# Performance work log

Measured on AMD Instinct MI355X. Metric: run time of the kernel, lower is better.

The kernel has to match this reference:

```python
import jax, jax.numpy as jnp
import numpy as np

B, H, S, D = 4, 16, 2048, 64


def setup_inputs() -> dict:
    key = jax.random.key(0)
    kq, kk, kv = jax.random.split(key, 3)
    q = jax.random.normal(kq, (B, H, S, D), dtype=jnp.float32)
    k = jax.random.normal(kk, (B, H, S, D), dtype=jnp.float32)
    v = jax.random.normal(kv, (B, H, S, D), dtype=jnp.float32)
    return {"q": q, "k": k, "v": v, "num_k": 170}


def reference(q, k, v, num_k):
    d_tensor = k.shape[-1]
    # [B,H,S,S] score matrix
    score = jnp.einsum("bhqd,bhkd->bhqk", q, k) / jnp.sqrt(jnp.float32(d_tensor))
    nk = min(int(num_k), k.shape[2])
    if nk:
        # kth-largest value per query row acts as threshold
        top_vals = jax.lax.top_k(score, nk)[0]          # [B,H,S,nk]
        thresh = top_vals[..., -1:]                      # [B,H,S,1]
        score = jnp.where(score < thresh, jnp.float32(-1e18), score)
    attn = jax.nn.softmax(score, axis=-1)
    return jnp.einsum("bhqk,bhkd->bhqd", attn, v)
```

## Files before the change

kernel.cpp:

```cpp
#include <hip/hip_runtime.h>
#include <math.h>

#define S_LEN 2048
#define DHEAD 64
#define NBINS 512
#define BPL (NBINS / 64)
#define CANDMAX 48
#define NBH 64
#define NROWS (NBH * S_LEN)
#define VT_BYTES (64ull * DHEAD * S_LEN * 2)

typedef _Float16 f16x8 __attribute__((ext_vector_type(8)));
typedef _Float16 f16x4 __attribute__((ext_vector_type(4)));
typedef float    f32x4 __attribute__((ext_vector_type(4)));

__global__ __launch_bounds__(256)
void prep_vt(const float* __restrict__ V, _Float16* __restrict__ VT) {
  const int bh  = (int)blockIdx.x >> 3;
  const int dg8 = (int)blockIdx.x & 7;
  const int t   = (int)threadIdx.x;
  const int dim = dg8 * 8 + (t >> 5);
  const int kc  = t & 31;
  const float* Vb = V + (size_t)bh * (S_LEN * DHEAD);
  _Float16* VTb = VT + ((size_t)bh * DHEAD + dim) * S_LEN;
  for (int i = 0; i < 8; ++i) {
    int key0 = (kc + i * 32) * 8;
    f16x8 h;
    #pragma unroll
    for (int j = 0; j < 8; ++j)
      h[j] = (_Float16)Vb[(size_t)(key0 + j) * DHEAD + dim];
    *(f16x8*)(VTb + key0) = h;
  }
}

__global__ __launch_bounds__(256, 4)
void qk_kernel(const float* __restrict__ Q, const float* __restrict__ K,
               float* __restrict__ Sws, int row0) {
  __shared__ __align__(16) char kbuf[32768];
  f16x8* Khw = (f16x8*)kbuf;
  f16x8* Klw = (f16x8*)(kbuf + 16384);

  const int tid  = (int)threadIdx.x;
  const int lane = tid & 63;
  const int wid  = tid >> 6;
  const int nxl  = (int)gridDim.x >> 3;
  const int xcd  = (int)blockIdx.x & 7;
  const int lb   = (int)blockIdx.x >> 3;
  const int rb   = lb >> 3;
  const int kb   = lb & 7;
  const int rowl = xcd * (nxl * 8) + rb * 64 + wid * 16;
  const int rowg = row0 + rowl;
  const int bh   = rowg >> 11;
  const int key0 = kb * 256;

  const int g = lane >> 4;
  const int m = lane & 15;

  f16x8 a_hi0, a_lo0, a_hi1, a_lo1;
  {
    const float* Qrow = Q + (size_t)(rowg + m) * DHEAD;
    float4 qa = *(const float4*)(Qrow + g * 8);
    float4 qb = *(const float4*)(Qrow + g * 8 + 4);
    float4 qc = *(const float4*)(Qrow + 32 + g * 8);
    float4 qd = *(const float4*)(Qrow + 32 + g * 8 + 4);
    float x[16] = {qa.x,qa.y,qa.z,qa.w, qb.x,qb.y,qb.z,qb.w,
                   qc.x,qc.y,qc.z,qc.w, qd.x,qd.y,qd.z,qd.w};
    #pragma unroll
    for (int j = 0; j < 8; ++j) {
      _Float16 h0 = (_Float16)x[j];
      a_hi0[j] = h0;  a_lo0[j] = (_Float16)(x[j] - (float)h0);
      _Float16 h1 = (_Float16)x[8 + j];
      a_hi1[j] = h1;  a_lo1[j] = (_Float16)(x[8 + j] - (float)h1);
    }
  }

  const float* Kb = K + (size_t)bh * (S_LEN * DHEAD);
  float* Srow = Sws + (size_t)rowl * S_LEN;

  const int skey  = tid >> 1;
  const int shalf = tid & 1;
  const int ssw   = skey & 7;

  float4 pf[8];
  {
    const float4* kr = (const float4*)(Kb + (size_t)(key0 + skey) * DHEAD + shalf * 32);
    #pragma unroll
    for (int j = 0; j < 8; ++j) pf[j] = kr[j];
  }

  #pragma unroll
  for (int t = 0; t < 2; ++t) {
    #pragma unroll
    for (int jj = 0; jj < 4; ++jj) {
      float x[8] = {pf[2*jj].x, pf[2*jj].y, pf[2*jj].z, pf[2*jj].w,
                    pf[2*jj+1].x, pf[2*jj+1].y, pf[2*jj+1].z, pf[2*jj+1].w};
      f16x8 hi, lo;
      #pragma unroll
      for (int j = 0; j < 8; ++j) {
        _Float16 h = (_Float16)x[j];
        hi[j] = h;
        lo[j] = (_Float16)(x[j] - (float)h);
      }
      int c = shalf * 4 + jj;
      Khw[skey * 8 + (c ^ ssw)] = hi;
      Klw[skey * 8 + (c ^ ssw)] = lo;
    }
    if (t + 1 < 2) {
      const float4* kr = (const float4*)(Kb + (size_t)(key0 + 128 + skey) * DHEAD + shalf * 32);
      #pragma unroll
      for (int j = 0; j < 8; ++j) pf[j] = kr[j];
    }
    __syncthreads();

    const f16x8* Kh = (const f16x8*)kbuf;
    const f16x8* Kl = (const f16x8*)(kbuf + 16384);
    int slot0 = ( g      ^ (m & 7));
    int slot1 = ((4 + g) ^ (m & 7));
    #pragma unroll
    for (int p = 0; p < 8; ++p) {
      int keyr = p * 16 + m;
      f16x8 b_hi0 = Kh[keyr * 8 + slot0];
      f16x8 b_hi1 = Kh[keyr * 8 + slot1];
      f16x8 b_lo0 = Kl[keyr * 8 + slot0];
      f16x8 b_lo1 = Kl[keyr * 8 + slot1];
      f32x4 acc = {0.f, 0.f, 0.f, 0.f};
      acc = __builtin_amdgcn_mfma_f32_16x16x32_f16(a_hi0, b_hi0, acc, 0, 0, 0);
      acc = __builtin_amdgcn_mfma_f32_16x16x32_f16(a_hi1, b_hi1, acc, 0, 0, 0);
      acc = __builtin_amdgcn_mfma_f32_16x16x32_f16(a_hi0, b_lo0, acc, 0, 0, 0);
      acc = __builtin_amdgcn_mfma_f32_16x16x32_f16(a_hi1, b_lo1, acc, 0, 0, 0);
      acc = __builtin_amdgcn_mfma_f32_16x16x32_f16(a_lo0, b_hi0, acc, 0, 0, 0);
      acc = __builtin_amdgcn_mfma_f32_16x16x32_f16(a_lo1, b_hi1, acc, 0, 0, 0);
      acc = __builtin_amdgcn_mfma_f32_16x16x32_f16(a_lo0, b_lo0, acc, 0, 0, 0);
      acc = __builtin_amdgcn_mfma_f32_16x16x32_f16(a_lo1, b_lo1, acc, 0, 0, 0);
      int col = key0 + t * 128 + p * 16 + m;
      #pragma unroll
      for (int rg = 0; rg < 4; ++rg)
        __builtin_nontemporal_store(acc[rg] * 0.125f,
            &Srow[(size_t)(g * 4 + rg) * S_LEN + col]);
    }
    __syncthreads();
  }
}

__global__ __launch_bounds__(512, 4)
void selmm_kernel(const float* __restrict__ Sws, const _Float16* __restrict__ VT,
                  const int* __restrict__ nkp, float* __restrict__ Out, int row0) {
  __shared__ unsigned histS[8][NBINS];
  __shared__ float candS[8][CANDMAX];
  __shared__ unsigned candCnt[8];
  __shared__ float psumS[16];
  __shared__ __align__(16) char pbuf[8192];
  __shared__ __align__(16) float4 redS[4][64];

  const int tid  = (int)threadIdx.x;
  const int lane = tid & 63;
  const int wid  = tid >> 6;
  const int nxl  = (int)gridDim.x >> 3;
  const int xcd  = (int)blockIdx.x & 7;
  const int lbk  = (int)blockIdx.x >> 3;
  const int rowlb = xcd * (nxl * 16) + lbk * 16;
  const int rowgb = row0 + rowlb;
  const int bh    = rowgb >> 11;

  int nk = nkp[0];
  if (nk > S_LEN) nk = S_LEN;

  unsigned* hw = histS[wid];
  float sarr[2][32];
  float thr2[2], vmx2[2];

  #pragma unroll
  for (int rr = 0; rr < 2; ++rr) {
    const int rloc = wid * 2 + rr;
    {
      const f32x4* S4 = (const f32x4*)(Sws + (size_t)(rowlb + rloc) * S_LEN);
      #pragma unroll
      for (int j = 0; j < 8; ++j) {
        f32x4 v4 = __builtin_nontemporal_load(S4 + j * 64 + lane);
        sarr[rr][j*4+0] = v4[0]; sarr[rr][j*4+1] = v4[1];
        sarr[rr][j*4+2] = v4[2]; sarr[rr][j*4+3] = v4[3];
      }
    }

    float vmax = -INFINITY, vmin = INFINITY;
    #pragma unroll
    for (int q = 0; q < 32; ++q) {
      vmax = fmaxf(vmax, sarr[rr][q]); vmin = fminf(vmin, sarr[rr][q]);
    }
    #pragma unroll
    for (int off = 32; off >= 1; off >>= 1) {
      vmax = fmaxf(vmax, __shfl_xor(vmax, off));
      vmin = fminf(vmin, __shfl_xor(vmin, off));
    }

    float thresh = -INFINITY;
    if (nk > 0) {
      float range = vmax - vmin;
      float scale = (range > 0.f) ? ((float)NBINS / range) : 0.f;
      float boff  = vmin * scale;

      #pragma unroll
      for (int i2 = 0; i2 < BPL; ++i2) hw[(i2 << 6) | lane] = 0u;
      #pragma unroll
      for (int q = 0; q < 32; ++q) {
        int bb = (int)fmaf(sarr[rr][q], scale, -boff);
        bb = bb < 0 ? 0 : (bb > NBINS - 1 ? NBINS - 1 : bb);
        atomicAdd(&hw[((bb & 7) << 6) | (bb >> 3)], 1u);
      }

      unsigned A = 0;
      #pragma unroll
      for (int i2 = 0; i2 < BPL; ++i2) A += hw[(i2 << 6) | lane];
      unsigned ssum = A;
      #pragma unroll
      for (int off = 1; off <= 32; off <<= 1) {
        unsigned u = (unsigned)__shfl_down((int)ssum, off);
        if (lane + off < 64) ssum += u;
      }
      unsigned cum = ssum - A;
      int bsel = -1; int mloc = 0; int nbloc = 0;
      #pragma unroll
      for (int i2 = BPL - 1; i2 >= 0; --i2) {
        unsigned c0 = cum; cum += hw[(i2 << 6) | lane];
        if (bsel < 0 && c0 < (unsigned)nk && cum >= (unsigned)nk) {
          bsel = (lane << 3) | i2; mloc = nk - (int)c0; nbloc = (int)(cum - c0);
        }
      }
      unsigned long long fm = __ballot(bsel >= 0);
      int srcl = __ffsll(fm) - 1;
      bsel = __shfl(bsel, srcl);
      int mth  = __shfl(mloc, srcl);
      int nbin = __shfl(nbloc, srcl);

      if (nbin <= CANDMAX) {
        if (lane == 0) candCnt[wid] = 0u;
        __builtin_amdgcn_wave_barrier();
        #pragma unroll
        for (int q = 0; q < 32; ++q) {
          int bb = (int)fmaf(sarr[rr][q], scale, -boff);
          bb = bb < 0 ? 0 : (bb > NBINS - 1 ? NBINS - 1 : bb);
          if (bb == bsel) {
            unsigned ix = atomicAdd(&candCnt[wid], 1u);
            if (ix < CANDMAX) candS[wid][ix] = sarr[rr][q];
          }
        }
        __builtin_amdgcn_wave_barrier();
        float prev = INFINITY, kth = -INFINITY;
        int got = 0, guard = 0;
        while (got < mth && guard++ <= CANDMAX) {
          float best = -INFINITY;
          for (int i = 0; i < nbin; ++i) {
            float v = candS[wid][i];
            if (v < prev && v > best) best = v;
          }
          int ce = 0;
          for (int i = 0; i < nbin; ++i) if (candS[wid][i] == best) ce++;
          got += ce; prev = best; kth = best;
        }
        thresh = kth;
      } else {
        unsigned inbin = 0;
        #pragma unroll
        for (int q = 0; q < 32; ++q) {
          int bb = (int)fmaf(sarr[rr][q], scale, -boff);
          bb = bb < 0 ? 0 : (bb > NBINS - 1 ? NBINS - 1 : bb);
          if (bb == bsel) inbin |= (1u << q);
        }
        while (true) {
          float cmax = -INFINITY;
          #pragma unroll
          for (int q = 0; q < 32; ++q) if (inbin & (1u << q)) cmax = fmaxf(cmax, sarr[rr][q]);
          #pragma unroll
          for (int off = 32; off >= 1; off >>= 1) cmax = fmaxf(cmax, __shfl_xor(cmax, off));
          int cnt = 0;
          #pragma unroll
          for (int q = 0; q < 32; ++q) if ((inbin & (1u << q)) && sarr[rr][q] == cmax) cnt++;
          #pragma unroll
          for (int off = 32; off >= 1; off >>= 1) cnt += __shfl_xor(cnt, off);
          if (mth <= cnt) { thresh = cmax; break; }
          mth -= cnt;
          #pragma unroll
          for (int q = 0; q < 32; ++q) if ((inbin & (1u << q)) && sarr[rr][q] == cmax) inbin &= ~(1u << q);
        }
      }
    }
    thr2[rr] = thresh; vmx2[rr] = vmax;

    float psum = 0.f;
    #pragma unroll
    for (int q = 0; q < 32; ++q) {
      float s = sarr[rr][q];
      psum += (s >= thresh) ? __expf(s - vmax) : 0.f;
    }
    #pragma unroll
    for (int off = 32; off >= 1; off >>= 1) psum += __shfl_xor(psum, off);
    if (lane == 0) psumS[rloc] = psum;
  }
  __syncthreads();

  const int g   = lane >> 4;
  const int n16 = lane & 15;
  const int dg  = wid & 3;
  const int kh  = wid >> 2;
  const _Float16* VTb = VT + (size_t)bh * (DHEAD * S_LEN);
  f32x4 acc = {0.f, 0.f, 0.f, 0.f};

  #pragma unroll
  for (int kt = 0; kt < 8; ++kt) {
    #pragma unroll
    for (int rr = 0; rr < 2; ++rr) {
      const int row = wid * 2 + rr;
      f16x4 pv;
      #pragma unroll
      for (int c = 0; c < 4; ++c) {
        float s = sarr[rr][kt * 4 + c];
        float p = (s >= thr2[rr]) ? __expf(s - vmx2[rr]) : 0.f;
        pv[c] = (_Float16)p;
      }
      *(f16x4*)(pbuf + ((row * 512 + lane * 8) ^ ((row & 7) << 4))) = pv;
    }
    __syncthreads();
    #pragma unroll
    for (int s = 0; s < 4; ++s) {
      f16x8 af = *(const f16x8*)(pbuf +
          ((n16 * 512 + kh * 256 + s * 64 + g * 16) ^ ((n16 & 7) << 4)));
      f16x8 bf = *(const f16x8*)(VTb + (size_t)(dg * 16 + n16) * S_LEN +
                                 kt * 256 + kh * 128 + s * 32 + g * 8);
      acc = __builtin_amdgcn_mfma_f32_16x16x32_f16(af, bf, acc, 0, 0, 0);
    }
    __syncthreads();
  }

  if (kh == 1) {
    redS[dg][lane] = make_float4(acc[0], acc[1], acc[2], acc[3]);
  }
  __syncthreads();
  if (kh == 0) {
    float4 o = redS[dg][lane];
    float ov[4] = {o.x, o.y, o.z, o.w};
    #pragma unroll
    for (int rg = 0; rg < 4; ++rg) {
      int row = g * 4 + rg;
      float val = (acc[rg] + ov[rg]) / psumS[row];
      Out[(size_t)(rowgb + row) * DHEAD + dg * 16 + n16] = val;
    }
  }
}

#define TQ 16
#define KT 128
#define NTILES (S_LEN / KT)
#define THREADS 512
#define LCAP 256
#define SOFF   0
#define KHI    131072
#define KLO    147456
#define HOFF   131072
#define KLOFF  147456
#define PLOFF  155648

__global__ __launch_bounds__(THREADS, 2)
void dpsa_kernel(const float* __restrict__ Q, const float* __restrict__ K,
                 const float* __restrict__ V, const int* __restrict__ nkp,
                 float* __restrict__ Out) {
  __shared__ __align__(16) char smem[163840];
  float* Sf = (float*)(smem + SOFF);

  const int tid  = (int)threadIdx.x;
  const int lane = tid & 63;
  const int wid  = tid >> 6;
  const int bid  = (int)blockIdx.x;
  const int bh   = bid >> 7;
  const int qblk = bid & 127;
  const size_t base = (size_t)bh * (size_t)(S_LEN * DHEAD);
  const float* Kbh = K + base;
  const float* Vbh = V + base;

  int nk = nkp[0];
  if (nk > S_LEN) nk = S_LEN;

  const int g = lane >> 4;
  const int m = lane & 15;

  f16x8 a_hi0, a_lo0, a_hi1, a_lo1;
  {
    const float* Qrow = Q + base + (size_t)(qblk * TQ + m) * DHEAD;
    float4 qa = *(const float4*)(Qrow + g * 8);
    float4 qb = *(const float4*)(Qrow + g * 8 + 4);
    float4 qc = *(const float4*)(Qrow + 32 + g * 8);
    float4 qd = *(const float4*)(Qrow + 32 + g * 8 + 4);
    float x[16] = {qa.x,qa.y,qa.z,qa.w, qb.x,qb.y,qb.z,qb.w,
                   qc.x,qc.y,qc.z,qc.w, qd.x,qd.y,qd.z,qd.w};
    #pragma unroll
    for (int j = 0; j < 8; ++j) {
      _Float16 h0 = (_Float16)x[j];
      a_hi0[j] = h0;  a_lo0[j] = (_Float16)(x[j] - (float)h0);
      _Float16 h1 = (_Float16)x[8 + j];
      a_hi1[j] = h1;  a_lo1[j] = (_Float16)(x[8 + j] - (float)h1);
    }
  }

  const f16x8* Kh = (const f16x8*)(smem + KHI);
  const f16x8* Kl = (const f16x8*)(smem + KLO);
  const int keyl = tid >> 2;
  const int q4i  = tid & 3;
  const int sw   = keyl & 7;

  float4 pf0, pf1, pf2, pf3;
  {
    const float4* Kg4 = (const float4*)Kbh;
    int idx = keyl * 16 + q4i * 4;
    pf0 = Kg4[idx]; pf1 = Kg4[idx + 1]; pf2 = Kg4[idx + 2]; pf3 = Kg4[idx + 3];
  }

  for (int t = 0; t < NTILES; ++t) {
    {
      float x[16] = {pf0.x,pf0.y,pf0.z,pf0.w, pf1.x,pf1.y,pf1.z,pf1.w,
                     pf2.x,pf2.y,pf2.z,pf2.w, pf3.x,pf3.y,pf3.z,pf3.w};
      f16x8 hi0, hi1, lo0, lo1;
      #pragma unroll
      for (int j = 0; j < 8; ++j) {
        _Float16 h0 = (_Float16)x[j];
        hi0[j] = h0;  lo0[j] = (_Float16)(x[j] - (float)h0);
        _Float16 h1 = (_Float16)x[8 + j];
        hi1[j] = h1;  lo1[j] = (_Float16)(x[8 + j] - (float)h1);
      }
      f16x8* KhwF = (f16x8*)(smem + KHI);
      f16x8* KlwF = (f16x8*)(smem + KLO);
      KhwF[keyl * 8 + ((q4i * 2)     ^ sw)] = hi0;
      KhwF[keyl * 8 + ((q4i * 2 + 1) ^ sw)] = hi1;
      KlwF[keyl * 8 + ((q4i * 2)     ^ sw)] = lo0;
      KlwF[keyl * 8 + ((q4i * 2 + 1) ^ sw)] = lo1;
    }
    if (t + 1 < NTILES) {
      const float4* Kg4 = (const float4*)(Kbh + (size_t)(t + 1) * (KT * DHEAD));
      int idx = keyl * 16 + q4i * 4;
      pf0 = Kg4[idx]; pf1 = Kg4[idx + 1]; pf2 = Kg4[idx + 2]; pf3 = Kg4[idx + 3];
    }
    __syncthreads();
    {
      int keyr = wid * 16 + m;
      int s0 = ( g      ^ (m & 7));
      int s1 = ((4 + g) ^ (m & 7));
      f16x8 b_hi0 = Kh[keyr * 8 + s0];
      f16x8 b_hi1 = Kh[keyr * 8 + s1];
      f16x8 b_lo0 = Kl[keyr * 8 + s0];
      f16x8 b_lo1 = Kl[keyr * 8 + s1];
      f32x4 acc = {0.f, 0.f, 0.f, 0.f};
      acc = __builtin_amdgcn_mfma_f32_16x16x32_f16(a_hi0, b_hi0, acc, 0, 0, 0);
      acc = __builtin_amdgcn_mfma_f32_16x16x32_f16(a_hi1, b_hi1, acc, 0, 0, 0);
      acc = __builtin_amdgcn_mfma_f32_16x16x32_f16(a_hi0, b_lo0, acc, 0, 0, 0);
      acc = __builtin_amdgcn_mfma_f32_16x16x32_f16(a_hi1, b_lo1, acc, 0, 0, 0);
      acc = __builtin_amdgcn_mfma_f32_16x16x32_f16(a_lo0, b_hi0, acc, 0, 0, 0);
      acc = __builtin_amdgcn_mfma_f32_16x16x32_f16(a_lo1, b_hi1, acc, 0, 0, 0);
      int keyabs = t * KT + wid * 16 + m;
      #pragma unroll
      for (int rg = 0; rg < 4; ++rg)
        Sf[(size_t)(g * 4 + rg) * S_LEN + keyabs] = acc[rg] * 0.125f;
    }
    __syncthreads();
  }

  unsigned* hw = (unsigned*)(smem + HOFF)  + wid * NBINS;
  unsigned* kl = (unsigned*)(smem + KLOFF) + wid * LCAP;
  float*    pl = (float*)(smem + PLOFF)    + wid * LCAP;
  const float4* S4 = (const float4*)(smem + SOFF);

  for (int rr = 0; rr < 2; ++rr) {
    const int row = wid * 2 + rr;
    float sarr[32];
    #pragma unroll
    for (int j = 0; j < 8; ++j) {
      float4 v4 = S4[row * (S_LEN / 4) + j * 64 + lane];
      sarr[j*4+0] = v4.x; sarr[j*4+1] = v4.y;
      sarr[j*4+2] = v4.z; sarr[j*4+3] = v4.w;
    }

    float vmax = -INFINITY, vmin = INFINITY;
    #pragma unroll
    for (int q = 0; q < 32; ++q) {
      vmax = fmaxf(vmax, sarr[q]); vmin = fminf(vmin, sarr[q]);
    }
    #pragma unroll
    for (int off = 32; off >= 1; off >>= 1) {
      vmax = fmaxf(vmax, __shfl_xor(vmax, off));
      vmin = fminf(vmin, __shfl_xor(vmin, off));
    }

    float thresh = -INFINITY;
    if (nk > 0) {
      float range = vmax - vmin;
      float scale = (range > 0.f) ? ((float)NBINS / range) : 0.f;
      #pragma unroll
      for (int i2 = 0; i2 < BPL; ++i2) hw[(i2 << 6) | lane] = 0u;
      #pragma unroll
      for (int q = 0; q < 32; ++q) {
        int bb = (int)((sarr[q] - vmin) * scale);
        bb = bb < 0 ? 0 : (bb > NBINS - 1 ? NBINS - 1 : bb);
        atomicAdd(&hw[((bb & 7) << 6) | (bb >> 3)], 1u);
      }
      unsigned A = 0; unsigned hv[BPL];
      #pragma unroll
      for (int i2 = 0; i2 < BPL; ++i2) { hv[i2] = hw[(i2 << 6) | lane]; A += hv[i2]; }
      unsigned ssum = A;
      #pragma unroll
      for (int off = 1; off <= 32; off <<= 1) {
        unsigned u = (unsigned)__shfl_down((int)ssum, off);
        if (lane + off < 64) ssum += u;
      }
      unsigned cum = ssum - A;
      int bsel = -1; int mloc = 0;
      #pragma unroll
      for (int i2 = BPL - 1; i2 >= 0; --i2) {
        unsigned c0 = cum; cum += hv[i2];
        if (bsel < 0 && c0 < (unsigned)nk && cum >= (unsigned)nk) {
          bsel = (lane << 3) | i2; mloc = nk - (int)c0;
        }
      }
      unsigned long long fmk = __ballot(bsel >= 0);
      int srcl = __ffsll(fmk) - 1;
      bsel = __shfl(bsel, srcl);
      int mth = __shfl(mloc, srcl);

      unsigned inbin = 0;
      #pragma unroll
      for (int q = 0; q < 32; ++q) {
        int bb = (int)((sarr[q] - vmin) * scale);
        bb = bb < 0 ? 0 : (bb > NBINS - 1 ? NBINS - 1 : bb);
        if (bb == bsel) inbin |= (1u << q);
      }
      while (true) {
        float cmax = -INFINITY;
        #pragma unroll
        for (int q = 0; q < 32; ++q) if (inbin & (1u << q)) cmax = fmaxf(cmax, sarr[q]);
        #pragma unroll
        for (int off = 32; off >= 1; off >>= 1) cmax = fmaxf(cmax, __shfl_xor(cmax, off));
        int cnt = 0;
        #pragma unroll
        for (int q = 0; q < 32; ++q) if ((inbin & (1u << q)) && sarr[q] == cmax) cnt++;
        #pragma unroll
        for (int off = 32; off >= 1; off >>= 1) cnt += __shfl_xor(cnt, off);
        if (mth <= cnt) { thresh = cmax; break; }
        mth -= cnt;
        #pragma unroll
        for (int q = 0; q < 32; ++q) if ((inbin & (1u << q)) && sarr[q] == cmax) inbin &= ~(1u << q);
      }
    }

    float psum = 0.f;
    #pragma unroll
    for (int q = 0; q < 32; ++q) {
      float p = (sarr[q] >= thresh) ? expf(sarr[q] - vmax) : 0.f;
      sarr[q] = p; psum += p;
    }
    #pragma unroll
    for (int off = 32; off >= 1; off >>= 1) psum += __shfl_xor(psum, off);

    unsigned nkept = 0;
    #pragma unroll
    for (int q = 0; q < 32; ++q) {
      bool keep = sarr[q] > 0.f;
      unsigned long long mk = __ballot(keep);
      if (keep) {
        unsigned idx = nkept + (unsigned)__popcll(mk & ((1ull << lane) - 1ull));
        if (idx < LCAP) {
          kl[idx] = (unsigned)((q >> 2) * 256 + lane * 4 + (q & 3));
          pl[idx] = sarr[q];
        }
      }
      nkept += (unsigned)__popcll(mk);
    }

    float acc0 = 0.f, acc1 = 0.f, acc2 = 0.f, acc3 = 0.f;
    if (nkept <= LCAP) {
      unsigned i = 0;
      for (; i + 4 <= nkept; i += 4) {
        acc0 = fmaf(pl[i+0], Vbh[(size_t)kl[i+0] * DHEAD + lane], acc0);
        acc1 = fmaf(pl[i+1], Vbh[(size_t)kl[i+1] * DHEAD + lane], acc1);
        acc2 = fmaf(pl[i+2], Vbh[(size_t)kl[i+2] * DHEAD + lane], acc2);
        acc3 = fmaf(pl[i+3], Vbh[(size_t)kl[i+3] * DHEAD + lane], acc3);
      }
      for (; i < nkept; ++i)
        acc0 = fmaf(pl[i], Vbh[(size_t)kl[i] * DHEAD + lane], acc0);
    } else {
      #pragma unroll
      for (int q = 0; q < 32; ++q) {
        for (int sl = 0; sl < 64; ++sl) {
          float pp = __shfl(sarr[q], sl);
          if (pp > 0.f)
            acc0 = fmaf(pp, Vbh[(size_t)((q >> 2) * 256 + sl * 4 + (q & 3)) * DHEAD + lane], acc0);
        }
      }
    }
    float accv = (acc0 + acc1) + (acc2 + acc3);
    Out[base + (size_t)(qblk * TQ + row) * DHEAD + lane] = accv / psum;
  }
}

extern "C" void kernel_launch(void* const* d_in, const int* in_sizes, int n_in,
                              void* d_out, int out_size, void* d_ws, size_t ws_size,
                              hipStream_t stream) {
  const float* q  = (const float*)d_in[0];
  const float* k  = (const float*)d_in[1];
  const float* v  = (const float*)d_in[2];
  const int*   nk = (const int*)d_in[3];
  float* out = (float*)d_out;

  size_t srem = (ws_size > VT_BYTES) ? (ws_size - VT_BYTES) : 0;
  size_t maxrows = srem / ((size_t)S_LEN * sizeof(float));
  long long chunk = (long long)(maxrows / 512) * 512;
  if (chunk > NROWS) chunk = NROWS;

  if (chunk >= 512) {
    _Float16* vt = (_Float16*)d_ws;
    float* sws = (float*)((char*)d_ws + VT_BYTES);
    prep_vt<<<dim3(512), dim3(256), 0, stream>>>(v, vt);
    for (int row0 = 0; row0 < NROWS; row0 += (int)chunk) {
      int rows = (NROWS - row0 < (int)chunk) ? (NROWS - row0) : (int)chunk;
      qk_kernel<<<dim3(rows / 8), dim3(256), 0, stream>>>(q, k, sws, row0);
      selmm_kernel<<<dim3(rows / 16), dim3(512), 0, stream>>>(sws, vt, nk, out, row0);
    }
  } else {
    dpsa_kernel<<<dim3(8192), dim3(THREADS), 0, stream>>>(q, k, v, nk, out);
  }
}
```

Baseline: 902.0 us.

## Fuse QK and selection kernels into one software-pipelined mixed launch with double-buffered scores

Merges the QK score kernel and the top-k selection/PV kernel into a single launch. In each launch, blocks compute selection for chunk i-1 while other blocks compute scores for chunk i, using two score buffers in alternation. The goal is to overlap the compute-heavy QK work with the memory- and latency-heavy selection work, and to cut the number of kernel launches and tail bubbles. The cost is a shared 32KB LDS carve-out and 512-thread blocks at occupancy hint 2, which could lower occupancy for the selection path. The scheme also needs the workspace to hold two chunk buffers.

```diff
diff --git a/kernel.cpp b/kernel.cpp
--- a/kernel.cpp
+++ b/kernel.cpp
@@ -33,139 +33,141 @@
   }
 }
 
-__global__ __launch_bounds__(256, 4)
-void qk_kernel(const float* __restrict__ Q, const float* __restrict__ K,
-               float* __restrict__ Sws, int row0) {
-  __shared__ __align__(16) char kbuf[32768];
-  f16x8* Khw = (f16x8*)kbuf;
-  f16x8* Klw = (f16x8*)(kbuf + 16384);
-
+__global__ __launch_bounds__(512, 2)
+void mix_kernel(const float* __restrict__ Q, const float* __restrict__ K,
+                const float* __restrict__ Sprev, float* __restrict__ Snext,
+                const _Float16* __restrict__ VT, const int* __restrict__ nkp,
+                float* __restrict__ Out, int rowSel0, int rowQk0,
+                int selB, int qkB) {
+  __shared__ __align__(16) char smem[32768];
+
+  const int bid  = (int)blockIdx.x;
   const int tid  = (int)threadIdx.x;
   const int lane = tid & 63;
   const int wid  = tid >> 6;
-  const int nxl  = (int)gridDim.x >> 3;
-  const int xcd  = (int)blockIdx.x & 7;
-  const int lb   = (int)blockIdx.x >> 3;
-  const int rb   = lb >> 3;
-  const int kb   = lb & 7;
-  const int rowl = xcd * (nxl * 8) + rb * 64 + wid * 16;
-  const int rowg = row0 + rowl;
-  const int bh   = rowg >> 11;
-  const int key0 = kb * 256;
-
   const int g = lane >> 4;
   const int m = lane & 15;
 
-  f16x8 a_hi0, a_lo0, a_hi1, a_lo1;
-  {
-    const float* Qrow = Q + (size_t)(rowg + m) * DHEAD;
-    float4 qa = *(const float4*)(Qrow + g * 8);
-    float4 qb = *(const float4*)(Qrow + g * 8 + 4);
-    float4 qc = *(const float4*)(Qrow + 32 + g * 8);
-    float4 qd = *(const float4*)(Qrow + 32 + g * 8 + 4);
-    float x[16] = {qa.x,qa.y,qa.z,qa.w, qb.x,qb.y,qb.z,qb.w,
-                   qc.x,qc.y,qc.z,qc.w, qd.x,qd.y,qd.z,qd.w};
-    #pragma unroll
-    for (int j = 0; j < 8; ++j) {
-      _Float16 h0 = (_Float16)x[j];
-      a_hi0[j] = h0;  a_lo0[j] = (_Float16)(x[j] - (float)h0);
-      _Float16 h1 = (_Float16)x[8 + j];
-      a_hi1[j] = h1;  a_lo1[j] = (_Float16)(x[8 + j] - (float)h1);
-    }
-  }
-
-  const float* Kb = K + (size_t)bh * (S_LEN * DHEAD);
-  float* Srow = Sws + (size_t)rowl * S_LEN;
-
-  const int skey  = tid >> 1;
-  const int shalf = tid & 1;
-  const int ssw   = skey & 7;
-
-  float4 pf[8];
-  {
-    const float4* kr = (const float4*)(Kb + (size_t)(key0 + skey) * DHEAD + shalf * 32);
-    #pragma unroll
-    for (int j = 0; j < 8; ++j) pf[j] = kr[j];
-  }
-
-  #pragma unroll
-  for (int t = 0; t < 2; ++t) {
-    #pragma unroll
-    for (int jj = 0; jj < 4; ++jj) {
-      float x[8] = {pf[2*jj].x, pf[2*jj].y, pf[2*jj].z, pf[2*jj].w,
-                    pf[2*jj+1].x, pf[2*jj+1].y, pf[2*jj+1].z, pf[2*jj+1].w};
-      f16x8 hi, lo;
-      #pragma unroll
-      for (int j = 0; j < 8; ++j) {
-        _Float16 h = (_Float16)x[j];
-        hi[j] = h;
-        lo[j] = (_Float16)(x[j] - (float)h);
-      }
-      int c = shalf * 4 + jj;
-      Khw[skey * 8 + (c ^ ssw)] = hi;
-      Klw[skey * 8 + (c ^ ssw)] = lo;
-    }
-    if (t + 1 < 2) {
-      const float4* kr = (const float4*)(Kb + (size_t)(key0 + 128 + skey) * DHEAD + shalf * 32);
-      #pragma unroll
-      for (int j = 0; j < 8; ++j) pf[j] = kr[j];
-    }
-    __syncthreads();
-
-    const f16x8* Kh = (const f16x8*)kbuf;
-    const f16x8* Kl = (const f16x8*)(kbuf + 16384);
-    int slot0 = ( g      ^ (m & 7));
-    int slot1 = ((4 + g) ^ (m & 7));
-    #pragma unroll
-    for (int p = 0; p < 8; ++p) {
-      int keyr = p * 16 + m;
-      f16x8 b_hi0 = Kh[keyr * 8 + slot0];
-      f16x8 b_hi1 = Kh[keyr * 8 + slot1];
-      f16x8 b_lo0 = Kl[keyr * 8 + slot0];
-      f16x8 b_lo1 = Kl[keyr * 8 + slot1];
-      f32x4 acc = {0.f, 0.f, 0.f, 0.f};
-      acc = __builtin_amdgcn_mfma_f32_16x16x32_f16(a_hi0, b_hi0, acc, 0, 0, 0);
-      acc = __builtin_amdgcn_mfma_f32_16x16x32_f16(a_hi1, b_hi1, acc, 0, 0, 0);
-      acc = __builtin_amdgcn_mfma_f32_16x16x32_f16(a_hi0, b_lo0, acc, 0, 0, 0);
-      acc = __builtin_amdgcn_mfma_f32_16x16x32_f16(a_hi1, b_lo1, acc, 0, 0, 0);
-      acc = __builtin_amdgcn_mfma_f32_16x16x32_f16(a_lo0, b_hi0, acc, 0, 0, 0);
-      acc = __builtin_amdgcn_mfma_f32_16x16x32_f16(a_lo1, b_hi1, acc, 0, 0, 0);
-      acc = __builtin_amdgcn_mfma_f32_16x16x32_f16(a_lo0, b_lo0, acc, 0, 0, 0);
-      acc = __builtin_amdgcn_mfma_f32_16x16x32_f16(a_lo1, b_lo1, acc, 0, 0, 0);
-      int col = key0 + t * 128 + p * 16 + m;
-      #pragma unroll
-      for (int rg = 0; rg < 4; ++rg)
-        __builtin_nontemporal_store(acc[rg] * 0.125f,
-            &Srow[(size_t)(g * 4 + rg) * S_LEN + col]);
-    }
-    __syncthreads();
-  }
-}
-
-__global__ __launch_bounds__(512, 4)
-void selmm_kernel(const float* __restrict__ Sws, const _Float16* __restrict__ VT,
-                  const int* __restrict__ nkp, float* __restrict__ Out, int row0) {
-  __shared__ unsigned histS[8][NBINS];
-  __shared__ float candS[8][CANDMAX];
-  __shared__ unsigned candCnt[8];
-  __shared__ float psumS[16];
-  __shared__ __align__(16) char pbuf[8192];
-  __shared__ __align__(16) float4 redS[4][64];
-
-  const int tid  = (int)threadIdx.x;
-  const int lane = tid & 63;
-  const int wid  = tid >> 6;
-  const int nxl  = (int)gridDim.x >> 3;
-  const int xcd  = (int)blockIdx.x & 7;
-  const int lbk  = (int)blockIdx.x >> 3;
-  const int rowlb = xcd * (nxl * 16) + lbk * 16;
-  const int rowgb = row0 + rowlb;
-  const int bh    = rowgb >> 11;
-
   int nk = nkp[0];
   if (nk > S_LEN) nk = S_LEN;
 
-  unsigned* hw = histS[wid];
+  if (bid >= selB) {
+    f16x8* Khw = (f16x8*)smem;
+    f16x8* Klw = (f16x8*)(smem + 16384);
+    const int local = bid - selB;
+    const int nxlq  = qkB >> 3;
+    const int xcd   = local & 7;
+    const int lb    = local >> 3;
+    const int rb    = lb >> 3;
+    const int kb    = lb & 7;
+    const int rowlB = xcd * (nxlq * 16) + rb * 128;
+    const int rowg  = rowQk0 + rowlB + wid * 16;
+    const int bh    = rowg >> 11;
+    const int key0  = kb * 256;
+
+    f16x8 a_hi0, a_lo0, a_hi1, a_lo1;
+    {
+      const float* Qrow = Q + (size_t)(rowg + m) * DHEAD;
+      float4 qa = *(const float4*)(Qrow + g * 8);
+      float4 qb = *(const float4*)(Qrow + g * 8 + 4);
+      float4 qc = *(const float4*)(Qrow + 32 + g * 8);
+      float4 qd = *(const float4*)(Qrow + 32 + g * 8 + 4);
+      float x[16] = {qa.x,qa.y,qa.z,qa.w, qb.x,qb.y,qb.z,qb.w,
+                     qc.x,qc.y,qc.z,qc.w, qd.x,qd.y,qd.z,qd.w};
+      #pragma unroll
+      for (int j = 0; j < 8; ++j) {
+        _Float16 h0 = (_Float16)x[j];
+        a_hi0[j] = h0;  a_lo0[j] = (_Float16)(x[j] - (float)h0);
+        _Float16 h1 = (_Float16)x[8 + j];
+        a_hi1[j] = h1;  a_lo1[j] = (_Float16)(x[8 + j] - (float)h1);
+      }
+    }
+
+    const float* Kb = K + (size_t)bh * (S_LEN * DHEAD);
+    float* Srow = Snext + (size_t)(rowlB + wid * 16) * S_LEN;
+
+    const int keyl = tid >> 2;
+    const int q4i  = tid & 3;
+    const int sw   = keyl & 7;
+
+    float4 pf0, pf1, pf2, pf3;
+    {
+      const float4* Kg4 = (const float4*)(Kb + (size_t)key0 * DHEAD);
+      int idx = keyl * 16 + q4i * 4;
+      pf0 = Kg4[idx]; pf1 = Kg4[idx+1]; pf2 = Kg4[idx+2]; pf3 = Kg4[idx+3];
+    }
+
+    #pragma unroll
+    for (int t = 0; t < 2; ++t) {
+      {
+        float x[16] = {pf0.x,pf0.y,pf0.z,pf0.w, pf1.x,pf1.y,pf1.z,pf1.w,
+                       pf2.x,pf2.y,pf2.z,pf2.w, pf3.x,pf3.y,pf3.z,pf3.w};
+        f16x8 hi0, hi1, lo0, lo1;
+        #pragma unroll
+        for (int j = 0; j < 8; ++j) {
+          _Float16 h0 = (_Float16)x[j];
+          hi0[j] = h0;  lo0[j] = (_Float16)(x[j] - (float)h0);
+          _Float16 h1 = (_Float16)x[8 + j];
+          hi1[j] = h1;  lo1[j] = (_Float16)(x[8 + j] - (float)h1);
+        }
+        Khw[keyl * 8 + ((q4i * 2)     ^ sw)] = hi0;
+        Khw[keyl * 8 + ((q4i * 2 + 1) ^ sw)] = hi1;
+        Klw[keyl * 8 + ((q4i * 2)     ^ sw)] = lo0;
+        Klw[keyl * 8 + ((q4i * 2 + 1) ^ sw)] = lo1;
+      }
+      if (t + 1 < 2) {
+        const float4* Kg4 = (const float4*)(Kb + (size_t)(key0 + 128) * DHEAD);
+        int idx = keyl * 16 + q4i * 4;
+        pf0 = Kg4[idx]; pf1 = Kg4[idx+1]; pf2 = Kg4[idx+2]; pf3 = Kg4[idx+3];
+      }
+      __syncthreads();
+
+      const f16x8* Kh = (const f16x8*)smem;
+      const f16x8* Kl = (const f16x8*)(smem + 16384);
+      int slot0 = ( g      ^ (m & 7));
+      int slot1 = ((4 + g) ^ (m & 7));
+      #pragma unroll
+      for (int p = 0; p < 8; ++p) {
+        int keyr = p * 16 + m;
+        f16x8 b_hi0 = Kh[keyr * 8 + slot0];
+        f16x8 b_hi1 = Kh[keyr * 8 + slot1];
+        f16x8 b_lo0 = Kl[keyr * 8 + slot0];
+        f16x8 b_lo1 = Kl[keyr * 8 + slot1];
+        f32x4 acc = {0.f, 0.f, 0.f, 0.f};
+        acc = __builtin_amdgcn_mfma_f32_16x16x32_f16(a_hi0, b_hi0, acc, 0, 0, 0);
+        acc = __builtin_amdgcn_mfma_f32_16x16x32_f16(a_hi1, b_hi1, acc, 0, 0, 0);
+        acc = __builtin_amdgcn_mfma_f32_16x16x32_f16(a_hi0, b_lo0, acc, 0, 0, 0);
+        acc = __builtin_amdgcn_mfma_f32_16x16x32_f16(a_hi1, b_lo1, acc, 0, 0, 0);
+        acc = __builtin_amdgcn_mfma_f32_16x16x32_f16(a_lo0, b_hi0, acc, 0, 0, 0);
+        acc = __builtin_amdgcn_mfma_f32_16x16x32_f16(a_lo1, b_hi1, acc, 0, 0, 0);
+        acc = __builtin_amdgcn_mfma_f32_16x16x32_f16(a_lo0, b_lo0, acc, 0, 0, 0);
+        acc = __builtin_amdgcn_mfma_f32_16x16x32_f16(a_lo1, b_lo1, acc, 0, 0, 0);
+        int col = key0 + t * 128 + p * 16 + m;
+        #pragma unroll
+        for (int rg = 0; rg < 4; ++rg)
+          __builtin_nontemporal_store(acc[rg] * 0.125f,
+              &Srow[(size_t)(g * 4 + rg) * S_LEN + col]);
+      }
+      __syncthreads();
+    }
+    return;
+  }
+
+  unsigned* histS  = (unsigned*)smem;
+  char*     pbuf   = smem + 16384;
+  float4*   redS   = (float4*)(smem + 24576);
+  float*    candS  = (float*)(smem + 28672);
+  unsigned* candCnt= (unsigned*)(smem + 30208);
+  float*    psumS  = (float*)(smem + 30240);
+
+  const int nxl  = selB >> 3;
+  const int xcd  = bid & 7;
+  const int lbk  = bid >> 3;
+  const int rowlb = xcd * (nxl * 16) + lbk * 16;
+  const int rowgb = rowSel0 + rowlb;
+  const int bh    = rowgb >> 11;
+
+  unsigned* hw = histS + wid * NBINS;
   float sarr[2][32];
   float thr2[2], vmx2[2];
 
@@ -173,7 +175,7 @@
   for (int rr = 0; rr < 2; ++rr) {
     const int rloc = wid * 2 + rr;
     {
-      const f32x4* S4 = (const f32x4*)(Sws + (size_t)(rowlb + rloc) * S_LEN);
+      const f32x4* S4 = (const f32x4*)(Sprev + (size_t)(rowlb + rloc) * S_LEN);
       #pragma unroll
       for (int j = 0; j < 8; ++j) {
         f32x4 v4 = __builtin_nontemporal_load(S4 + j * 64 + lane);
@@ -241,7 +243,7 @@
           bb = bb < 0 ? 0 : (bb > NBINS - 1 ? NBINS - 1 : bb);
           if (bb == bsel) {
             unsigned ix = atomicAdd(&candCnt[wid], 1u);
-            if (ix < CANDMAX) candS[wid][ix] = sarr[rr][q];
+            if (ix < CANDMAX) candS[wid * CANDMAX + ix] = sarr[rr][q];
           }
         }
         __builtin_amdgcn_wave_barrier();
@@ -250,11 +252,11 @@
         while (got < mth && guard++ <= CANDMAX) {
           float best = -INFINITY;
           for (int i = 0; i < nbin; ++i) {
-            float v = candS[wid][i];
+            float v = candS[wid * CANDMAX + i];
             if (v < prev && v > best) best = v;
           }
           int ce = 0;
-          for (int i = 0; i < nbin; ++i) if (candS[wid][i] == best) ce++;
+          for (int i = 0; i < nbin; ++i) if (candS[wid * CANDMAX + i] == best) ce++;
           got += ce; prev = best; kth = best;
         }
         thresh = kth;
@@ -298,7 +300,6 @@
   }
   __syncthreads();
 
-  const int g   = lane >> 4;
   const int n16 = lane & 15;
   const int dg  = wid & 3;
   const int kh  = wid >> 2;
@@ -332,11 +333,11 @@
   }
 
   if (kh == 1) {
-    redS[dg][lane] = make_float4(acc[0], acc[1], acc[2], acc[3]);
+    redS[dg * 64 + lane] = make_float4(acc[0], acc[1], acc[2], acc[3]);
   }
   __syncthreads();
   if (kh == 0) {
-    float4 o = redS[dg][lane];
+    float4 o = redS[dg * 64 + lane];
     float ov[4] = {o.x, o.y, o.z, o.w};
     #pragma unroll
     for (int rg = 0; rg < 4; ++rg) {
@@ -607,18 +608,29 @@
   float* out = (float*)d_out;
 
   size_t srem = (ws_size > VT_BYTES) ? (ws_size - VT_BYTES) : 0;
-  size_t maxrows = srem / ((size_t)S_LEN * sizeof(float));
-  long long chunk = (long long)(maxrows / 512) * 512;
-  if (chunk > NROWS) chunk = NROWS;
-
-  if (chunk >= 512) {
+  size_t maxChunk = srem / 2 / ((size_t)S_LEN * sizeof(float));
+  int chunk = 0;
+  if (maxChunk >= 1024) {
+    chunk = 1024;
+    while ((size_t)(chunk * 2) <= maxChunk && chunk * 2 <= 4096) chunk *= 2;
+  }
+
+  if (chunk >= 1024) {
     _Float16* vt = (_Float16*)d_ws;
-    float* sws = (float*)((char*)d_ws + VT_BYTES);
+    float* sbuf0 = (float*)((char*)d_ws + VT_BYTES);
+    float* sbuf1 = sbuf0 + (size_t)chunk * S_LEN;
+    int nch = NROWS / chunk;
     prep_vt<<<dim3(512), dim3(256), 0, stream>>>(v, vt);
-    for (int row0 = 0; row0 < NROWS; row0 += (int)chunk) {
-      int rows = (NROWS - row0 < (int)chunk) ? (NROWS - row0) : (int)chunk;
-      qk_kernel<<<dim3(rows / 8), dim3(256), 0, stream>>>(q, k, sws, row0);
-      selmm_kernel<<<dim3(rows / 16), dim3(512), 0, stream>>>(sws, vt, nk, out, row0);
+    for (int i = 0; i <= nch; ++i) {
+      int qkRows  = (i < nch) ? chunk : 0;
+      int selRows = (i > 0) ? chunk : 0;
+      int qkB  = qkRows / 16;
+      int selB = selRows / 16;
+      float* Snext = (i & 1) ? sbuf1 : sbuf0;
+      float* Sprev = (i & 1) ? sbuf0 : sbuf1;
+      mix_kernel<<<dim3(selB + qkB), dim3(512), 0, stream>>>(
+          q, k, Sprev, Snext, vt, nk, out,
+          (i - 1) * chunk, i * chunk, selB, qkB);
     }
   } else {
     dpsa_kernel<<<dim3(8192), dim3(THREADS), 0, stream>>>(q, k, v, nk, out);
```

After: 1.174 ms. 30.1% more time.
